# Optimization experiments

Hardware: AMD Instinct MI355X
Metric: run time of the kernel (lower is better)

Reference implementation:

```python
import jax, jax.numpy as jnp
import numpy as np

N_NODES = 50000
N_EDGES = 1600000


def _gcn_conv(x, src, dst, W, b, num_nodes):
    # PyG GCNConv: out = D^-1/2 (A + I) D^-1/2 (x W) + b
    h = x @ W  # transform first (in_channels >= out_channels)
    deg = jax.ops.segment_sum(jnp.ones_like(dst, dtype=h.dtype), dst,
                              num_segments=num_nodes)
    dinv = jax.lax.rsqrt(deg)  # deg >= 1 thanks to self-loops
    norm = dinv[src] * dinv[dst]  # [E+N]
    msg = h[src] * norm[:, None]  # gather + scale
    out = jax.ops.segment_sum(msg, dst, num_segments=num_nodes)
    return out + b


def setup_inputs() -> dict:
    key = jax.random.key(0)
    k1, k2, k3, k4 = jax.random.split(key, 4)
    x = jax.random.normal(k1, (N_NODES, 512), dtype=jnp.float32)
    edge_index = jax.random.randint(k2, (2, N_EDGES), 0, N_NODES, dtype=jnp.int64)
    # Glorot-ish init for the two GCNConv weights
    W1 = jax.random.normal(k3, (512, 128), dtype=jnp.float32) * (1.0 / np.sqrt(512))
    b1 = jnp.zeros((128,), dtype=jnp.float32)
    W2 = jax.random.normal(k4, (128, 64), dtype=jnp.float32) * (1.0 / np.sqrt(128))
    b2 = jnp.zeros((64,), dtype=jnp.float32)
    return {"x": x, "edge_index": edge_index, "W1": W1, "b1": b1,
            "W2": W2, "b2": b2}


def reference(x, edge_index, W1, b1, W2, b2):
    num_nodes = x.shape[0]
    loop = jnp.arange(num_nodes, dtype=edge_index.dtype)
    src = jnp.concatenate([edge_index[0], loop])  # add self-loops
    dst = jnp.concatenate([edge_index[1], loop])
    h = jax.nn.relu(_gcn_conv(x, src, dst, W1, b1, num_nodes))
    out = _gcn_conv(h, src, dst, W2, b2, num_nodes)
    return out
```

## Files before the change

### kernel.cpp

```cpp
#include <hip/hip_runtime.h>
#include <hip/hip_bf16.h>


typedef __attribute__((ext_vector_type(8))) short short8;
typedef __attribute__((ext_vector_type(4))) float f32x4;

#define BSHIFT 9
#define BSIZE 512
constexpr int NBMAX = 128;
constexpr int CAP = 32768;
constexpr int CHUNK = 4096;

__device__ __forceinline__ unsigned short bf16_bits(float f) {
  __hip_bfloat16 h = __float2bfloat16(f);
  return *(unsigned short*)&h;
}
__device__ __forceinline__ float bf16_f(unsigned short u) {
  __hip_bfloat16 h = *(__hip_bfloat16*)&u;
  return __bfloat162float(h);
}

__device__ __forceinline__ int edge_at(const void* p, long long i, int is64) {
  return is64 ? (int)((const long long*)p)[i] : ((const int*)p)[i];
}

__global__ void k_detect(const int* __restrict__ w, int* flag, int nwords,
                         int* __restrict__ ccur, int NB) {
  __shared__ int nz;
  if (threadIdx.x == 0) nz = 0;
  __syncthreads();
  for (int i = 1 + 2 * (int)threadIdx.x; i < nwords; i += 2 * (int)blockDim.x)
    if (w[i] != 0) nz = 1;
  if ((int)threadIdx.x < NB) ccur[threadIdx.x] = (int)threadIdx.x * CAP;
  __syncthreads();
  if (threadIdx.x == 0) *flag = (nz == 0) ? 1 : 0;
}

__global__ __launch_bounds__(256) void k_binA(
    const void* __restrict__ eidx, const int* __restrict__ flag,
    int* __restrict__ ccur, unsigned* __restrict__ pairs, int E, int NB) {
  __shared__ int cnt[NBMAX];
  __shared__ int scn[NBMAX + 1];
  __shared__ int cur[NBMAX];
  __shared__ int gbase[NBMAX];
  __shared__ unsigned out[CHUNK];
  const int is64 = *flag;
  const int tid = threadIdx.x;
  const int cs = blockIdx.x * CHUNK;
  const int n = min(CHUNK, E - cs);
  for (int b = tid; b < NB; b += 256) cnt[b] = 0;
  __syncthreads();
  unsigned pk[CHUNK / 256];
#pragma unroll
  for (int it = 0; it < CHUNK / 256; ++it) {
    int i = cs + it * 256 + tid;
    unsigned p = 0xFFFFFFFFu;
    if (i < E) {
      int s = edge_at(eidx, i, is64);
      int d = edge_at(eidx, (long long)E + i, is64);
      p = ((unsigned)d << 16) | (unsigned)s;
      atomicAdd(&cnt[d >> BSHIFT], 1);
    }
    pk[it] = p;
  }
  __syncthreads();
  if (tid < NB) scn[tid + 1] = cnt[tid];
  if (tid == 0) scn[0] = 0;
  __syncthreads();
  for (int off = 1; off < NB; off <<= 1) {
    int t = 0;
    if (tid < NB && tid + 1 > off) t = scn[tid + 1 - off];
    __syncthreads();
    if (tid < NB && tid + 1 > off) scn[tid + 1] += t;
    __syncthreads();
  }
  if (tid < NB) {
    cur[tid] = scn[tid];
    gbase[tid] = (cnt[tid] > 0) ? atomicAdd(&ccur[tid], cnt[tid]) : 0;
  }
  __syncthreads();
#pragma unroll
  for (int it = 0; it < CHUNK / 256; ++it) {
    unsigned p = pk[it];
    if (p != 0xFFFFFFFFu) {
      int b = (int)(p >> (16 + BSHIFT));
      int pos = atomicAdd(&cur[b], 1);
      out[pos] = p;
    }
  }
  __syncthreads();
  for (int p2 = tid; p2 < n; p2 += 256) {
    unsigned v = out[p2];
    int b = (int)(v >> (16 + BSHIFT));
    pairs[gbase[b] + (p2 - scn[b])] = v;
  }
}

__global__ __launch_bounds__(128) void k_scanb(
    const int* __restrict__ ccur, int* __restrict__ bbase,
    int* __restrict__ rowptr, int NB, int N, int E) {
  __shared__ int buf[NBMAX];
  int tid = threadIdx.x;
  int v = (tid < NB) ? (ccur[tid] - tid * CAP) : 0;
  buf[tid] = v;
  __syncthreads();
  for (int off = 1; off < NBMAX; off <<= 1) {
    int t = (tid >= off) ? buf[tid - off] : 0;
    __syncthreads();
    buf[tid] += t;
    __syncthreads();
  }
  if (tid < NB) bbase[tid] = buf[tid] - v;
  if (tid == 0) rowptr[N] = E;
}

__global__ __launch_bounds__(256) void k_binB(
    const unsigned* __restrict__ pairs, const int* __restrict__ ccur,
    const int* __restrict__ bbase, int* __restrict__ rowptr,
    float* __restrict__ dinv, int* __restrict__ elist, int N) {
  __shared__ int hist[BSIZE];
  __shared__ int loc[BSIZE];
  const int b = blockIdx.x;
  const int tid = threadIdx.x;
  const int nbeg = b * CAP;
  const int cntb = ccur[b] - nbeg;
  const int base = bbase[b];
  const int j0 = tid, j1 = tid + 256;
  hist[j0] = 0; hist[j1] = 0;
  __syncthreads();
  for (int i = tid; i < cntb; i += 256) {
    unsigned v = pairs[nbeg + i];
    atomicAdd(&hist[(v >> 16) & (BSIZE - 1)], 1);
  }
  __syncthreads();
  loc[j0] = hist[j0]; loc[j1] = hist[j1];
  __syncthreads();
  for (int off = 1; off < BSIZE; off <<= 1) {
    int v0 = (j0 >= off) ? loc[j0 - off] : 0;
    int v1 = (j1 >= off) ? loc[j1 - off] : 0;
    __syncthreads();
    loc[j0] += v0; loc[j1] += v1;
    __syncthreads();
  }
  int c0 = base + loc[j0] - hist[j0];
  int c1 = base + loc[j1] - hist[j1];
  int gd0 = b * BSIZE + j0, gd1 = b * BSIZE + j1;
  if (gd0 < N) { rowptr[gd0] = c0; dinv[gd0] = rsqrtf((float)(hist[j0] + 1)); }
  if (gd1 < N) { rowptr[gd1] = c1; dinv[gd1] = rsqrtf((float)(hist[j1] + 1)); }
  __syncthreads();
  hist[j0] = c0; hist[j1] = c1;
  __syncthreads();
  for (int i = tid; i < cntb; i += 256) {
    unsigned v = pairs[nbeg + i];
    int p = atomicAdd(&hist[(v >> 16) & (BSIZE - 1)], 1);
    elist[p] = (int)(v & 0xFFFFu);
  }
}

__global__ void k_prepw(const float* __restrict__ W, unsigned short* __restrict__ Whi,
                        unsigned short* __restrict__ Wlo, int K, int N) {
  int o = blockIdx.x * blockDim.x + threadIdx.x;
  if (o >= K * N) return;
  int n = o / K, k = o % K;
  float w = W[(long long)k * N + n];
  unsigned short hb = bf16_bits(w);
  unsigned short lb = bf16_bits(w - bf16_f(hb));
  Whi[o] = hb;
  Wlo[o] = lb;
}

template <int K, int NOUT, int WX>
__global__ __launch_bounds__(256) void k_gemm_mfma(
    const float* __restrict__ X, const unsigned short* __restrict__ Whi,
    const unsigned short* __restrict__ Wlo, const float* __restrict__ dinv,
    unsigned short* __restrict__ Hs, int M) {
  constexpr int WY = 4 / WX;
  constexpr int BM = 64 * WY;
  constexpr int BN = 64 * WX;
  constexpr int KC = 32;
  constexpr int KP = 40;
  static_assert(BN == NOUT, "block covers full N");
  __shared__ unsigned short Ah[BM][KP], Al[BM][KP];
  __shared__ unsigned short Bh[BN][KP], Bl[BN][KP];
  const int tid = threadIdx.x;
  const int lane = tid & 63, wv = tid >> 6;
  const int wy = wv / WX, wx = wv % WX;
  const int fm = lane & 15;
  const int fq = lane >> 4;
  const int base = blockIdx.x * BM;

  f32x4 acc[4][4];
#pragma unroll
  for (int i = 0; i < 4; ++i)
#pragma unroll
    for (int j = 0; j < 4; ++j) acc[i][j] = (f32x4){0.f, 0.f, 0.f, 0.f};

  for (int k0 = 0; k0 < K; k0 += KC) {
    __syncthreads();
#pragma unroll
    for (int it = 0; it < BM / 32; ++it) {
      int chunk = tid + it * 256;
      int r = chunk >> 3, c = chunk & 7;
      float4 v = make_float4(0.f, 0.f, 0.f, 0.f);
      if (base + r < M) v = *(const float4*)&X[(long long)(base + r) * K + k0 + c * 4];
      ushort4 hv, lv;
      hv.x = bf16_bits(v.x); lv.x = bf16_bits(v.x - bf16_f(hv.x));
      hv.y = bf16_bits(v.y); lv.y = bf16_bits(v.y - bf16_f(hv.y));
      hv.z = bf16_bits(v.z); lv.z = bf16_bits(v.z - bf16_f(hv.z));
      hv.w = bf16_bits(v.w); lv.w = bf16_bits(v.w - bf16_f(hv.w));
      *(ushort4*)&Ah[r][c * 4] = hv;
      *(ushort4*)&Al[r][c * 4] = lv;
    }
#pragma unroll
    for (int it = 0; it < (BN * 4 + 255) / 256; ++it) {
      int chunk = tid + it * 256;
      if (chunk < BN * 4) {
        int n = chunk >> 2, cc = chunk & 3;
        *(uint4*)&Bh[n][cc * 8] = *(const uint4*)&Whi[(long long)n * K + k0 + cc * 8];
        *(uint4*)&Bl[n][cc * 8] = *(const uint4*)&Wlo[(long long)n * K + k0 + cc * 8];
      }
    }
    __syncthreads();
    short8 ah[4], al[4], bh[4], bl[4];
#pragma unroll
    for (int i = 0; i < 4; ++i) {
      ah[i] = *(short8*)&Ah[wy * 64 + i * 16 + fm][fq * 8];
      al[i] = *(short8*)&Al[wy * 64 + i * 16 + fm][fq * 8];
      bh[i] = *(short8*)&Bh[wx * 64 + i * 16 + fm][fq * 8];
      bl[i] = *(short8*)&Bl[wx * 64 + i * 16 + fm][fq * 8];
    }
#pragma unroll
    for (int i = 0; i < 4; ++i)
#pragma unroll
      for (int j = 0; j < 4; ++j) {
        acc[i][j] = __builtin_amdgcn_mfma_f32_16x16x32_bf16(ah[i], bh[j], acc[i][j], 0, 0, 0);
        acc[i][j] = __builtin_amdgcn_mfma_f32_16x16x32_bf16(ah[i], bl[j], acc[i][j], 0, 0, 0);
        acc[i][j] = __builtin_amdgcn_mfma_f32_16x16x32_bf16(al[i], bh[j], acc[i][j], 0, 0, 0);
      }
  }
#pragma unroll
  for (int i = 0; i < 4; ++i) {
#pragma unroll
    for (int reg = 0; reg < 4; ++reg) {
      int row = base + wy * 64 + i * 16 + fq * 4 + reg;
      if (row < M) {
        float dv = dinv[row];
#pragma unroll
        for (int j = 0; j < 4; ++j)
          Hs[(long long)row * NOUT + wx * 64 + j * 16 + fm] =
              bf16_bits(acc[i][j][reg] * dv);
      }
    }
  }
}

__device__ __forceinline__ void acc8(float* a, uint4 u) {
  const unsigned* p = (const unsigned*)&u;
#pragma unroll
  for (int q = 0; q < 4; ++q) {
    unsigned w = p[q];
    a[2 * q]     += __uint_as_float(w << 16);
    a[2 * q + 1] += __uint_as_float(w & 0xFFFF0000u);
  }
}

template <int C, bool RELU>
__global__ __launch_bounds__(256) void k_gather(
    const int* __restrict__ rowptr, const int* __restrict__ elist,
    const float* __restrict__ dinv, const unsigned short* __restrict__ Hs,
    const float* __restrict__ bias, float* __restrict__ OUT, int N) {
  constexpr int TPN = C / 8;
  constexpr int NPB = 256 / TPN;
  const int node = blockIdx.x * NPB + (int)threadIdx.x / TPN;
  const int lane = (int)threadIdx.x % TPN;
  if (node >= N) return;
  const int col = lane * 8;
  const int beg = rowptr[node];
  const int end = rowptr[node + 1];
  float a0[8] = {0, 0, 0, 0, 0, 0, 0, 0};
  float a1[8] = {0, 0, 0, 0, 0, 0, 0, 0};
  acc8(a0, *(const uint4*)&Hs[(long long)node * C + col]);
  int e = beg;
  for (; e + 3 < end; e += 4) {
    int s0 = elist[e], s1 = elist[e + 1], s2 = elist[e + 2], s3 = elist[e + 3];
    uint4 v0 = *(const uint4*)&Hs[(long long)s0 * C + col];
    uint4 v1 = *(const uint4*)&Hs[(long long)s1 * C + col];
    uint4 v2 = *(const uint4*)&Hs[(long long)s2 * C + col];
    uint4 v3 = *(const uint4*)&Hs[(long long)s3 * C + col];
    acc8(a0, v0); acc8(a1, v1); acc8(a0, v2); acc8(a1, v3);
  }
  for (; e < end; ++e) {
    uint4 v0 = *(const uint4*)&Hs[(long long)elist[e] * C + col];
    acc8(a0, v0);
  }
  const float dv = dinv[node];
  float o[8];
#pragma unroll
  for (int i = 0; i < 8; ++i) {
    o[i] = (a0[i] + a1[i]) * dv + bias[col + i];
    if (RELU) o[i] = fmaxf(o[i], 0.f);
  }
  *(float4*)&OUT[(long long)node * C + col] = make_float4(o[0], o[1], o[2], o[3]);
  *(float4*)&OUT[(long long)node * C + col + 4] = make_float4(o[4], o[5], o[6], o[7]);
}

extern "C" void kernel_launch(void* const* d_in, const int* in_sizes, int n_in,
                              void* d_out, int out_size, void* d_ws, size_t ws_size,
                              hipStream_t stream) {
  const float* x  = (const float*)d_in[0];
  const void*  ei = d_in[1];
  const float* W1 = (const float*)d_in[2];
  const float* b1 = (const float*)d_in[3];
  const float* W2 = (const float*)d_in[4];
  const float* b2 = (const float*)d_in[5];
  float* out = (float*)d_out;
  const int N = in_sizes[0] / 512;
  const int E = in_sizes[1] / 2;
  const int NB = (N + BSIZE - 1) >> BSHIFT;

  char* ws = (char*)d_ws;
  size_t off = 0;
  auto take = [&](size_t bytes) {
    void* p = ws + off;
    off = (off + bytes + 255) & ~(size_t)255;
    return p;
  };
  float* dinv   = (float*)take((size_t)N * 4);
  int*   flag   = (int*)take(4);
  int*   rowptr = (int*)take((size_t)(N + 1) * 4);
  int*   ccur   = (int*)take((size_t)NBMAX * 4);
  int*   bbase  = (int*)take((size_t)NBMAX * 4);
  int*   elist  = (int*)take((size_t)E * 4);
  unsigned short* Wt1h = (unsigned short*)take((size_t)512 * 128 * 2);
  unsigned short* Wt1l = (unsigned short*)take((size_t)512 * 128 * 2);
  unsigned short* Wt2h = (unsigned short*)take((size_t)128 * 64 * 2);
  unsigned short* Wt2l = (unsigned short*)take((size_t)128 * 64 * 2);
  unsigned short* Hs = (unsigned short*)take((size_t)N * 128 * 2);
  float* h2     = (float*)take((size_t)N * 128 * 4);
  unsigned short* Hs2 = Hs;
  unsigned* pairs = (unsigned*)h2;

  const int B = 256;
  k_detect<<<1, B, 0, stream>>>((const int*)ei, flag, 2048, ccur, NB);
  k_binA<<<(E + CHUNK - 1) / CHUNK, B, 0, stream>>>(ei, flag, ccur, pairs, E, NB);
  k_scanb<<<1, 128, 0, stream>>>(ccur, bbase, rowptr, NB, N, E);
  k_binB<<<NB, B, 0, stream>>>(pairs, ccur, bbase, rowptr, dinv, elist, N);
  k_prepw<<<(512 * 128 + B - 1) / B, B, 0, stream>>>(W1, Wt1h, Wt1l, 512, 128);
  k_prepw<<<(128 * 64 + B - 1) / B, B, 0, stream>>>(W2, Wt2h, Wt2l, 128, 64);
  k_gemm_mfma<512, 128, 2><<<(N + 127) / 128, B, 0, stream>>>(x, Wt1h, Wt1l, dinv, Hs, N);
  k_gather<128, true><<<(N + 15) / 16, B, 0, stream>>>(rowptr, elist, dinv, Hs, b1, h2, N);
  k_gemm_mfma<128, 64, 1><<<(N + 255) / 256, B, 0, stream>>>(h2, Wt2h, Wt2l, dinv, Hs2, N);
  k_gather<64, false><<<(N + 31) / 32, B, 0, stream>>>(rowptr, elist, dinv, Hs2, b2, out, N);
}
```

Measured before the change: 373.2 us.

## Use direct global-to-LDS loads for weights and shrink GEMM row tiles

Weight tiles are now copied into shared memory with the global_load_lds builtin, which skips staging them through registers. The row padding on the LDS arrays is removed so the direct-load layout is contiguous. The per-wave M tile shrinks from 64 to 32 rows, which halves block height, doubles the grid and lowers accumulator register pressure. Dropping the padding may add LDS bank conflicts on the fragment reads, and smaller tiles re-read the weights more often.

```diff
diff --git a/kernel.cpp b/kernel.cpp
--- a/kernel.cpp
+++ b/kernel.cpp
@@ -18,6 +18,12 @@
 __device__ __forceinline__ float bf16_f(unsigned short u) {
   __hip_bfloat16 h = *(__hip_bfloat16*)&u;
   return __bfloat162float(h);
+}
+
+__device__ __forceinline__ void gload_lds16(const void* g, void* l) {
+  __builtin_amdgcn_global_load_lds(
+      (const __attribute__((address_space(1))) unsigned*)g,
+      (__attribute__((address_space(3))) unsigned*)l, 16, 0, 0);
 }
 
 __device__ __forceinline__ int edge_at(const void* p, long long i, int is64) {
@@ -169,19 +175,20 @@
   Wlo[o] = lb;
 }
 
-template <int K, int NOUT, int WX>
+template <int K, int NOUT, int WM, int WY, int WX>
 __global__ __launch_bounds__(256) void k_gemm_mfma(
     const float* __restrict__ X, const unsigned short* __restrict__ Whi,
     const unsigned short* __restrict__ Wlo, const float* __restrict__ dinv,
     unsigned short* __restrict__ Hs, int M) {
-  constexpr int WY = 4 / WX;
-  constexpr int BM = 64 * WY;
+  constexpr int BM = WM * WY;
   constexpr int BN = 64 * WX;
   constexpr int KC = 32;
-  constexpr int KP = 40;
+  constexpr int I = WM / 16;
+  static_assert(WY * WX == 4, "4 waves");
   static_assert(BN == NOUT, "block covers full N");
-  __shared__ unsigned short Ah[BM][KP], Al[BM][KP];
-  __shared__ unsigned short Bh[BN][KP], Bl[BN][KP];
+  static_assert((BN * 4) % 256 == 0, "B chunk count divisible by block");
+  __shared__ unsigned short Ah[BM][KC], Al[BM][KC];
+  __shared__ unsigned short Bh[BN][KC], Bl[BN][KC];
   const int tid = threadIdx.x;
   const int lane = tid & 63, wv = tid >> 6;
   const int wy = wv / WX, wx = wv % WX;
@@ -189,9 +196,9 @@
   const int fq = lane >> 4;
   const int base = blockIdx.x * BM;
 
-  f32x4 acc[4][4];
-#pragma unroll
-  for (int i = 0; i < 4; ++i)
+  f32x4 acc[I][4];
+#pragma unroll
+  for (int i = 0; i < I; ++i)
 #pragma unroll
     for (int j = 0; j < 4; ++j) acc[i][j] = (f32x4){0.f, 0.f, 0.f, 0.f};
 
@@ -212,25 +219,28 @@
       *(ushort4*)&Al[r][c * 4] = lv;
     }
 #pragma unroll
-    for (int it = 0; it < (BN * 4 + 255) / 256; ++it) {
-      int chunk = tid + it * 256;
-      if (chunk < BN * 4) {
-        int n = chunk >> 2, cc = chunk & 3;
-        *(uint4*)&Bh[n][cc * 8] = *(const uint4*)&Whi[(long long)n * K + k0 + cc * 8];
-        *(uint4*)&Bl[n][cc * 8] = *(const uint4*)&Wlo[(long long)n * K + k0 + cc * 8];
-      }
-    }
-    __syncthreads();
-    short8 ah[4], al[4], bh[4], bl[4];
-#pragma unroll
-    for (int i = 0; i < 4; ++i) {
-      ah[i] = *(short8*)&Ah[wy * 64 + i * 16 + fm][fq * 8];
-      al[i] = *(short8*)&Al[wy * 64 + i * 16 + fm][fq * 8];
-      bh[i] = *(short8*)&Bh[wx * 64 + i * 16 + fm][fq * 8];
-      bl[i] = *(short8*)&Bl[wx * 64 + i * 16 + fm][fq * 8];
-    }
-#pragma unroll
-    for (int i = 0; i < 4; ++i)
+    for (int it = 0; it < (BN * 4) / 256; ++it) {
+      int cb = it * 256 + wv * 64;
+      int chunk = cb + lane;
+      int n = chunk >> 2, cc = chunk & 3;
+      const long long go = (long long)n * K + k0 + cc * 8;
+      gload_lds16(&Whi[go], (unsigned short*)Bh + (size_t)cb * 8);
+      gload_lds16(&Wlo[go], (unsigned short*)Bl + (size_t)cb * 8);
+    }
+    __syncthreads();
+    short8 ah[I], al[I], bh[4], bl[4];
+#pragma unroll
+    for (int i = 0; i < I; ++i) {
+      ah[i] = *(short8*)&Ah[wy * WM + i * 16 + fm][fq * 8];
+      al[i] = *(short8*)&Al[wy * WM + i * 16 + fm][fq * 8];
+    }
+#pragma unroll
+    for (int j = 0; j < 4; ++j) {
+      bh[j] = *(short8*)&Bh[wx * 64 + j * 16 + fm][fq * 8];
+      bl[j] = *(short8*)&Bl[wx * 64 + j * 16 + fm][fq * 8];
+    }
+#pragma unroll
+    for (int i = 0; i < I; ++i)
 #pragma unroll
       for (int j = 0; j < 4; ++j) {
         acc[i][j] = __builtin_amdgcn_mfma_f32_16x16x32_bf16(ah[i], bh[j], acc[i][j], 0, 0, 0);
@@ -239,10 +249,10 @@
       }
   }
 #pragma unroll
-  for (int i = 0; i < 4; ++i) {
+  for (int i = 0; i < I; ++i) {
 #pragma unroll
     for (int reg = 0; reg < 4; ++reg) {
-      int row = base + wy * 64 + i * 16 + fq * 4 + reg;
+      int row = base + wy * WM + i * 16 + fq * 4 + reg;
       if (row < M) {
         float dv = dinv[row];
 #pragma unroll
@@ -347,8 +357,10 @@
   k_binB<<<NB, B, 0, stream>>>(pairs, ccur, bbase, rowptr, dinv, elist, N);
   k_prepw<<<(512 * 128 + B - 1) / B, B, 0, stream>>>(W1, Wt1h, Wt1l, 512, 128);
   k_prepw<<<(128 * 64 + B - 1) / B, B, 0, stream>>>(W2, Wt2h, Wt2l, 128, 64);
-  k_gemm_mfma<512, 128, 2><<<(N + 127) / 128, B, 0, stream>>>(x, Wt1h, Wt1l, dinv, Hs, N);
+  k_gemm_mfma<512, 128, 32, 2, 2><<<(N + 63) / 64, B, 0, stream>>>(
+      x, Wt1h, Wt1l, dinv, Hs, N);
   k_gather<128, true><<<(N + 15) / 16, B, 0, stream>>>(rowptr, elist, dinv, Hs, b1, h2, N);
-  k_gemm_mfma<128, 64, 1><<<(N + 255) / 256, B, 0, stream>>>(h2, Wt2h, Wt2l, dinv, Hs2, N);
+  k_gemm_mfma<128, 64, 32, 4, 1><<<(N + 127) / 128, B, 0, stream>>>(
+      h2, Wt2h, Wt2l, dinv, Hs2, N);
   k_gather<64, false><<<(N + 31) / 32, B, 0, stream>>>(rowptr, elist, dinv, Hs2, b2, out, N);
 }
```

After: 350.5 us. 1.06x faster.
